# Kernel tuning notes

Measured on AMD Instinct MI355X. Metric: run time of the kernel, lower is better.

Reference implementation:

```python
import jax, jax.numpy as jnp
import numpy as np

DIM = 1024
NUM_HEADS = 16
HEAD_DIM = DIM // NUM_HEADS
SCALE = HEAD_DIM ** -0.5


def setup_inputs() -> dict:
    key = jax.random.key(0)
    ks = jax.random.split(key, 9)
    s = 0.02
    return {
        "x": jax.random.normal(ks[0], (4, 2048, DIM), dtype=jnp.float32),
        "Wq": jax.random.normal(ks[1], (DIM, DIM), dtype=jnp.float32) * s,
        "bq": jax.random.normal(ks[2], (DIM,), dtype=jnp.float32) * s,
        "Wk": jax.random.normal(ks[3], (DIM, DIM), dtype=jnp.float32) * s,
        "bk": jax.random.normal(ks[4], (DIM,), dtype=jnp.float32) * s,
        "Wv": jax.random.normal(ks[5], (DIM, DIM), dtype=jnp.float32) * s,
        "bv": jax.random.normal(ks[6], (DIM,), dtype=jnp.float32) * s,
        "Wo": jax.random.normal(ks[7], (DIM, DIM), dtype=jnp.float32) * s,
        "bo": jax.random.normal(ks[8], (DIM,), dtype=jnp.float32) * s,
    }


def reference(x, Wq, bq, Wk, bk, Wv, bv, Wo, bo):
    B, S, D = x.shape
    H, Dh = NUM_HEADS, HEAD_DIM

    def heads(t):  # [B,S,D] -> [B,H,S,Dh]
        return t.reshape(B, S, H, Dh).transpose(0, 2, 1, 3)

    q = heads(x @ Wq.T + bq)
    k = heads(x @ Wk.T + bk)
    v = heads(x @ Wv.T + bv)

    attn = jnp.einsum('bnqd,bnkd->bnqk', q, k) * SCALE
    attn = jax.nn.softmax(attn, axis=-1)
    out = jnp.einsum('bnqk,bnkd->bnqd', attn, v)  # [B,H,S,Dh]
    out = out.transpose(0, 2, 1, 3).reshape(B, S, D)
    return out @ Wo.T + bo
```

## Files before the change

kernel.cpp:

```cpp
#include <hip/hip_runtime.h>
#include <stdint.h>

#define DIMD 1024
#define NH   16
#define DH   64
#define BB   4
#define SS   2048
#define MTOT 8192

static constexpr float QSCALE = 0.18033688011112042f;

typedef unsigned short u16;
typedef __attribute__((ext_vector_type(8))) short bf8;
typedef __attribute__((ext_vector_type(4))) float f4;
typedef __attribute__((ext_vector_type(16))) float f16v;

#if __has_builtin(__builtin_amdgcn_exp2f)
#define EXP2(x) __builtin_amdgcn_exp2f(x)
#else
#define EXP2(x) exp2f(x)
#endif

__device__ inline u16 f2bf(float f) {
    union { float f; uint32_t u; } v; v.f = f;
    uint32_t r = v.u + 0x7fffu + ((v.u >> 16) & 1u);
    return (u16)(r >> 16);
}

__device__ inline void gld16(const void* g, void* l) {
    __builtin_amdgcn_global_load_lds(
        (const __attribute__((address_space(1))) uint32_t*)g,
        (__attribute__((address_space(3))) uint32_t*)l, 16, 0, 0);
}

__device__ inline uint32_t cvtpk(float lo, float hi) {
    uint32_t r;
    asm("v_cvt_pk_bf16_f32 %0, %1, %2" : "=v"(r) : "v"(lo), "v"(hi));
    return r;
}

__global__ void cvt_bf16(const float* __restrict__ src, u16* __restrict__ dst, int n) {
    int i = (blockIdx.x * blockDim.x + threadIdx.x) * 4;
    if (i >= n) return;
    float4 v = *(const float4*)(src + i);
    ushort4 o;
    o.x = f2bf(v.x); o.y = f2bf(v.y); o.z = f2bf(v.z); o.w = f2bf(v.w);
    *(ushort4*)(dst + i) = o;
}

__global__ __launch_bounds__(256, 2) void gemm_qkv(
    const u16* __restrict__ xb, const u16* __restrict__ Wb,
    const float* __restrict__ bq, const float* __restrict__ bk, const float* __restrict__ bv,
    u16* __restrict__ qkv, u16* __restrict__ vtb)
{
    __shared__ u16 lA[128 * 64];
    __shared__ u16 lB[128 * 64];
    const int tid = threadIdx.x;
    const int bm = blockIdx.x, bn = blockIdx.y, z = blockIdx.z;
    const u16* W = Wb + (size_t)z * DIMD * DIMD;
    const float* bias = (z == 0) ? bq : ((z == 1) ? bk : bv);
    u16* outp = qkv + (size_t)z * (size_t)MTOT * DIMD;

    const int lane = tid & 63, w = tid >> 6;
    const int wr = (w >> 1) * 64, wc = (w & 1) * 64;
    f4 acc[4][4] = {};

    const char* Abase = (const char*)xb + (size_t)(bm * 128) * 2048;
    const char* Bbase = (const char*)W + (size_t)(bn * 128) * 2048;

    for (int kt = 0; kt < 16; ++kt) {
        __syncthreads();
        #pragma unroll
        for (int p = 0; p < 4; ++p) {
            int off = (p * 256 + tid) * 16;
            int row = off >> 7, cb = off & 127;
            int scb = cb ^ ((row & 7) << 4);
            gld16(Abase + (size_t)row * 2048 + kt * 128 + scb, (char*)lA + off);
            gld16(Bbase + (size_t)row * 2048 + kt * 128 + scb, (char*)lB + off);
        }
        __syncthreads();
        #pragma unroll
        for (int ks = 0; ks < 2; ++ks) {
            const int cb = ks * 64 + ((lane >> 4) << 4);
            bf8 af[4], bfr[4];
            #pragma unroll
            for (int mi = 0; mi < 4; ++mi) {
                int r = wr + mi * 16 + (lane & 15);
                af[mi] = *(const bf8*)((const char*)lA + r * 128 + (cb ^ ((r & 7) << 4)));
            }
            #pragma unroll
            for (int ni = 0; ni < 4; ++ni) {
                int r = wc + ni * 16 + (lane & 15);
                bfr[ni] = *(const bf8*)((const char*)lB + r * 128 + (cb ^ ((r & 7) << 4)));
            }
            #pragma unroll
            for (int mi = 0; mi < 4; ++mi)
                #pragma unroll
                for (int ni = 0; ni < 4; ++ni)
                    acc[mi][ni] = __builtin_amdgcn_mfma_f32_16x16x32_bf16(af[mi], bfr[ni], acc[mi][ni], 0, 0, 0);
        }
    }

    if (z == 2) {
        #pragma unroll
        for (int ni = 0; ni < 4; ++ni) {
            int col = bn * 128 + wc + ni * 16 + (lane & 15);
            float bi = bias[col];
            int h = col >> 6, dh = col & 63;
            #pragma unroll
            for (int mi = 0; mi < 4; ++mi) {
                int row0 = bm * 128 + wr + mi * 16 + ((lane >> 4) << 2);
                int b = row0 >> 11, s = row0 & 2047;
                ushort4 st;
                st.x = f2bf(acc[mi][ni][0] + bi);
                st.y = f2bf(acc[mi][ni][1] + bi);
                st.z = f2bf(acc[mi][ni][2] + bi);
                st.w = f2bf(acc[mi][ni][3] + bi);
                *(ushort4*)(vtb + ((size_t)(b * NH + h) * DH + dh) * SS + s) = st;
            }
        }
    } else {
        const float mulv = (z == 0) ? QSCALE : 1.0f;
        #pragma unroll
        for (int ni = 0; ni < 4; ++ni) {
            int col = bn * 128 + wc + ni * 16 + (lane & 15);
            float bi = bias[col];
            int h = col >> 6, dh = col & 63;
            #pragma unroll
            for (int mi = 0; mi < 4; ++mi) {
                #pragma unroll
                for (int r = 0; r < 4; ++r) {
                    int row = bm * 128 + wr + mi * 16 + ((lane >> 4) << 2) + r;
                    int b = row >> 11, s = row & 2047;
                    outp[(((size_t)(b * NH + h) * SS + s) << 6) + dh] = f2bf((acc[mi][ni][r] + bi) * mulv);
                }
            }
        }
    }
}

__global__ __launch_bounds__(256, 2) void gemm_out(
    const u16* __restrict__ Ab, const u16* __restrict__ Wo,
    const float* __restrict__ bo, float* __restrict__ dout)
{
    __shared__ u16 lA[128 * 64];
    __shared__ u16 lB[128 * 64];
    const int tid = threadIdx.x;
    const int bm = blockIdx.x, bn = blockIdx.y;
    const int lane = tid & 63, w = tid >> 6;
    const int wr = (w >> 1) * 64, wc = (w & 1) * 64;
    f4 acc[4][4] = {};
    const char* Abase = (const char*)Ab + (size_t)(bm * 128) * 2048;
    const char* Bbase = (const char*)Wo + (size_t)(bn * 128) * 2048;

    for (int kt = 0; kt < 16; ++kt) {
        __syncthreads();
        #pragma unroll
        for (int p = 0; p < 4; ++p) {
            int off = (p * 256 + tid) * 16;
            int row = off >> 7, cb = off & 127;
            int scb = cb ^ ((row & 7) << 4);
            gld16(Abase + (size_t)row * 2048 + kt * 128 + scb, (char*)lA + off);
            gld16(Bbase + (size_t)row * 2048 + kt * 128 + scb, (char*)lB + off);
        }
        __syncthreads();
        #pragma unroll
        for (int ks = 0; ks < 2; ++ks) {
            const int cb = ks * 64 + ((lane >> 4) << 4);
            bf8 af[4], bfr[4];
            #pragma unroll
            for (int mi = 0; mi < 4; ++mi) {
                int r = wr + mi * 16 + (lane & 15);
                af[mi] = *(const bf8*)((const char*)lA + r * 128 + (cb ^ ((r & 7) << 4)));
            }
            #pragma unroll
            for (int ni = 0; ni < 4; ++ni) {
                int r = wc + ni * 16 + (lane & 15);
                bfr[ni] = *(const bf8*)((const char*)lB + r * 128 + (cb ^ ((r & 7) << 4)));
            }
            #pragma unroll
            for (int mi = 0; mi < 4; ++mi)
                #pragma unroll
                for (int ni = 0; ni < 4; ++ni)
                    acc[mi][ni] = __builtin_amdgcn_mfma_f32_16x16x32_bf16(af[mi], bfr[ni], acc[mi][ni], 0, 0, 0);
        }
    }
    #pragma unroll
    for (int ni = 0; ni < 4; ++ni) {
        int col = bn * 128 + wc + ni * 16 + (lane & 15);
        float bi = bo[col];
        #pragma unroll
        for (int mi = 0; mi < 4; ++mi) {
            #pragma unroll
            for (int r = 0; r < 4; ++r) {
                int row = bm * 128 + wr + mi * 16 + ((lane >> 4) << 2) + r;
                dout[(size_t)row * DIMD + col] = acc[mi][ni][r] + bi;
            }
        }
    }
}

__global__ __launch_bounds__(512, 2) void attn_fwd(
    const u16* __restrict__ Q, const u16* __restrict__ K,
    const u16* __restrict__ Vt, u16* __restrict__ O)
{
    __shared__ u16 lK[2][64 * 64];
    __shared__ u16 lV[2][64 * 64];

    const int tid = threadIdx.x;
    const int lane = tid & 63, w = tid >> 6;
    const int hi = lane >> 5, l31 = lane & 31;
    const int bh = blockIdx.y;
    const int qb0 = blockIdx.x * 256;
    const char* Kbase = (const char*)(K + (size_t)bh * SS * DH);
    const char* Vbase = (const char*)(Vt + (size_t)bh * DH * SS);

    const int qrow = qb0 + w * 32 + l31;
    const u16* Qp = Q + (size_t)bh * SS * DH + (size_t)qrow * DH;
    bf8 qf[4];
    #pragma unroll
    for (int kd = 0; kd < 4; ++kd)
        qf[kd] = *(const bf8*)(Qp + kd * 16 + hi * 8);

    f16v oacc0 = {}, oacc1 = {};
    float lsum = 0.f;

    auto stage = [&](int buf, int kv0) {
        int off = tid * 16;
        int row = off >> 7, cb = off & 127;
        int scb = cb ^ ((row & 7) << 4);
        gld16(Kbase + (size_t)(kv0 + row) * 128 + scb, (char*)lK[buf] + off);
        gld16(Vbase + (size_t)row * (SS * 2) + (size_t)kv0 * 2 + scb, (char*)lV[buf] + off);
    };

    stage(0, 0);
    __syncthreads();

    for (int it = 0; it < SS / 64; ++it) {
        const int cur = it & 1;
        if (it + 1 < SS / 64) stage(cur ^ 1, (it + 1) * 64);

        const char* lKc = (const char*)lK[cur];
        const char* lVc = (const char*)lV[cur];

        f16v s0 = {}, s1 = {};
        __builtin_amdgcn_s_setprio(1);
        #pragma unroll
        for (int kd = 0; kd < 4; ++kd) {
            const int colb = 32 * kd + 16 * hi;
            const int r0 = l31, r1 = 32 + l31;
            bf8 kf0 = *(const bf8*)(lKc + r0 * 128 + (colb ^ ((r0 & 7) << 4)));
            bf8 kf1 = *(const bf8*)(lKc + r1 * 128 + (colb ^ ((r1 & 7) << 4)));
            s0 = __builtin_amdgcn_mfma_f32_32x32x16_bf16(kf0, qf[kd], s0, 0, 0, 0);
            s1 = __builtin_amdgcn_mfma_f32_32x32x16_bf16(kf1, qf[kd], s1, 0, 0, 0);
        }
        __builtin_amdgcn_s_setprio(0);

        float ps[16];
        #pragma unroll
        for (int i = 0; i < 16; ++i) {
            float e0 = EXP2(s0[i]);
            float e1 = EXP2(s1[i]);
            s0[i] = e0; s1[i] = e1;
            ps[i] = e0 + e1;
        }
        float t0 = (ps[0] + ps[1]) + (ps[2] + ps[3]);
        float t1 = (ps[4] + ps[5]) + (ps[6] + ps[7]);
        float t2 = (ps[8] + ps[9]) + (ps[10] + ps[11]);
        float t3 = (ps[12] + ps[13]) + (ps[14] + ps[15]);
        lsum += (t0 + t1) + (t2 + t3);

        uint32_t wv0[8], wv1[8];
        #pragma unroll
        for (int a = 0; a < 4; ++a) {
            wv0[a * 2 + 0] = cvtpk(s0[4 * a + 0], s0[4 * a + 1]);
            wv0[a * 2 + 1] = cvtpk(s0[4 * a + 2], s0[4 * a + 3]);
            wv1[a * 2 + 0] = cvtpk(s1[4 * a + 0], s1[4 * a + 1]);
            wv1[a * 2 + 1] = cvtpk(s1[4 * a + 2], s1[4 * a + 3]);
        }

        #pragma unroll
        for (int ks = 0; ks < 4; ++ks) {
            const int kss = ks & 1;
            const uint32_t* wv = (ks < 2) ? wv0 : wv1;
            uint32_t w0 = wv[(2 * kss) * 2 + 0];
            uint32_t w1 = wv[(2 * kss) * 2 + 1];
            uint32_t w2 = wv[(2 * kss + 1) * 2 + 0];
            uint32_t w3 = wv[(2 * kss + 1) * 2 + 1];
            asm("v_permlane32_swap_b32 %0, %1" : "+v"(w0), "+v"(w2));
            asm("v_permlane32_swap_b32 %0, %1" : "+v"(w1), "+v"(w3));
            union { uint32_t u[4]; bf8 v; } pb;
            pb.u[0] = w0; pb.u[1] = w1; pb.u[2] = w2; pb.u[3] = w3;

            const int colb = 32 * ks + 16 * hi;
            const int r0 = l31, r1 = 32 + l31;
            bf8 vf0 = *(const bf8*)(lVc + r0 * 128 + (colb ^ ((r0 & 7) << 4)));
            bf8 vf1 = *(const bf8*)(lVc + r1 * 128 + (colb ^ ((r1 & 7) << 4)));
            __builtin_amdgcn_s_setprio(1);
            oacc0 = __builtin_amdgcn_mfma_f32_32x32x16_bf16(vf0, pb.v, oacc0, 0, 0, 0);
            oacc1 = __builtin_amdgcn_mfma_f32_32x32x16_bf16(vf1, pb.v, oacc1, 0, 0, 0);
            __builtin_amdgcn_s_setprio(0);
        }

        __syncthreads();
    }

    const float l = lsum + __shfl_xor(lsum, 32, 64);
    const int b = bh >> 4, h = bh & 15;
    const float inv = 1.f / l;
    u16* orow = O + (((size_t)(b * SS + qrow)) << 10) + h * DH;
    #pragma unroll
    for (int g = 0; g < 4; ++g) {
        ushort4 st0, st1;
        st0.x = f2bf(oacc0[4 * g + 0] * inv); st0.y = f2bf(oacc0[4 * g + 1] * inv);
        st0.z = f2bf(oacc0[4 * g + 2] * inv); st0.w = f2bf(oacc0[4 * g + 3] * inv);
        st1.x = f2bf(oacc1[4 * g + 0] * inv); st1.y = f2bf(oacc1[4 * g + 1] * inv);
        st1.z = f2bf(oacc1[4 * g + 2] * inv); st1.w = f2bf(oacc1[4 * g + 3] * inv);
        *(ushort4*)(orow + 8 * g + 4 * hi) = st0;
        *(ushort4*)(orow + 32 + 8 * g + 4 * hi) = st1;
    }
}

extern "C" void kernel_launch(void* const* d_in, const int* in_sizes, int n_in,
                              void* d_out, int out_size, void* d_ws, size_t ws_size,
                              hipStream_t stream) {
    const float* x  = (const float*)d_in[0];
    const float* Wq = (const float*)d_in[1];
    const float* bq = (const float*)d_in[2];
    const float* Wk = (const float*)d_in[3];
    const float* bk = (const float*)d_in[4];
    const float* Wv = (const float*)d_in[5];
    const float* bv = (const float*)d_in[6];
    const float* Wo = (const float*)d_in[7];
    const float* bo = (const float*)d_in[8];
    float* out = (float*)d_out;

    u16* wsp = (u16*)d_ws;
    const size_t NX = (size_t)MTOT * DIMD;
    const size_t NW = (size_t)DIMD * DIMD;
    u16* xb   = wsp;
    u16* Wb   = wsp + NX;
    u16* Qb   = wsp + NX + 4 * NW;
    u16* Kb   = Qb + NX;
    u16* Vtb  = Kb + NX;
    u16* attn = xb;

    cvt_bf16<<<dim3((int)(NX / 4 / 256)), 256, 0, stream>>>(x, xb, (int)NX);
    cvt_bf16<<<dim3((int)(NW / 4 / 256)), 256, 0, stream>>>(Wq, Wb + 0 * NW, (int)NW);
    cvt_bf16<<<dim3((int)(NW / 4 / 256)), 256, 0, stream>>>(Wk, Wb + 1 * NW, (int)NW);
    cvt_bf16<<<dim3((int)(NW / 4 / 256)), 256, 0, stream>>>(Wv, Wb + 2 * NW, (int)NW);
    cvt_bf16<<<dim3((int)(NW / 4 / 256)), 256, 0, stream>>>(Wo, Wb + 3 * NW, (int)NW);

    gemm_qkv<<<dim3(MTOT / 128, DIMD / 128, 3), 256, 0, stream>>>(xb, Wb, bq, bk, bv, Qb, Vtb);
    attn_fwd<<<dim3(SS / 256, BB * NH), 512, 0, stream>>>(Qb, Kb, Vtb, attn);
    gemm_out<<<dim3(MTOT / 128, DIMD / 128), 256, 0, stream>>>(attn, Wb + 3 * NW, bo, out);
}
```

Baseline: 185.7 us.

## Enlarge GEMM tiles with double-buffered LDS pipeline and give attention waves 64 query rows

```diff
diff --git a/kernel.cpp b/kernel.cpp
--- a/kernel.cpp
+++ b/kernel.cpp
@@ -20,6 +20,12 @@
 #else
 #define EXP2(x) exp2f(x)
 #endif
+
+#define SCHED0() __builtin_amdgcn_sched_barrier(0)
+#define BAR()  { SCHED0(); __builtin_amdgcn_s_barrier(); SCHED0(); }
+#define VM8()  { asm volatile("s_waitcnt vmcnt(8)" ::: "memory"); SCHED0(); }
+#define VM6()  { asm volatile("s_waitcnt vmcnt(6)" ::: "memory"); SCHED0(); }
+#define VM0()  { asm volatile("s_waitcnt vmcnt(0)" ::: "memory"); SCHED0(); }
 
 __device__ inline u16 f2bf(float f) {
     union { float f; uint32_t u; } v; v.f = f;
@@ -48,68 +54,112 @@
     *(ushort4*)(dst + i) = o;
 }
 
-__global__ __launch_bounds__(256, 2) void gemm_qkv(
+__global__ __launch_bounds__(512, 2) void gemm_qkv(
     const u16* __restrict__ xb, const u16* __restrict__ Wb,
     const float* __restrict__ bq, const float* __restrict__ bk, const float* __restrict__ bv,
     u16* __restrict__ qkv, u16* __restrict__ vtb)
 {
-    __shared__ u16 lA[128 * 64];
-    __shared__ u16 lB[128 * 64];
-    const int tid = threadIdx.x;
-    const int bm = blockIdx.x, bn = blockIdx.y, z = blockIdx.z;
+    __shared__ __align__(16) u16 lds[2][2][256 * 64];
+
+    int flat = blockIdx.x + 32 * blockIdx.y + 128 * blockIdx.z;
+    int swz = (flat & 7) * 48 + (flat >> 3);
+    int bm = swz & 31;
+    int j = swz >> 5;
+    int bn = j & 3, z = j >> 2;
+
     const u16* W = Wb + (size_t)z * DIMD * DIMD;
     const float* bias = (z == 0) ? bq : ((z == 1) ? bk : bv);
     u16* outp = qkv + (size_t)z * (size_t)MTOT * DIMD;
 
+    const int tid = threadIdx.x;
     const int lane = tid & 63, w = tid >> 6;
-    const int wr = (w >> 1) * 64, wc = (w & 1) * 64;
-    f4 acc[4][4] = {};
-
-    const char* Abase = (const char*)xb + (size_t)(bm * 128) * 2048;
-    const char* Bbase = (const char*)W + (size_t)(bn * 128) * 2048;
-
-    for (int kt = 0; kt < 16; ++kt) {
-        __syncthreads();
+    const int wr = (w >> 2) * 128, wc = (w & 3) * 64;
+
+    const char* Abase = (const char*)xb + (size_t)(bm * 256) * 2048;
+    const char* Bbase = (const char*)W + (size_t)(bn * 256) * 2048;
+
+    auto stage = [&](int t, int buf) {
         #pragma unroll
         for (int p = 0; p < 4; ++p) {
-            int off = (p * 256 + tid) * 16;
+            int off = (p * 512 + tid) * 16;
             int row = off >> 7, cb = off & 127;
             int scb = cb ^ ((row & 7) << 4);
-            gld16(Abase + (size_t)row * 2048 + kt * 128 + scb, (char*)lA + off);
-            gld16(Bbase + (size_t)row * 2048 + kt * 128 + scb, (char*)lB + off);
-        }
-        __syncthreads();
-        #pragma unroll
-        for (int ks = 0; ks < 2; ++ks) {
-            const int cb = ks * 64 + ((lane >> 4) << 4);
-            bf8 af[4], bfr[4];
-            #pragma unroll
-            for (int mi = 0; mi < 4; ++mi) {
-                int r = wr + mi * 16 + (lane & 15);
-                af[mi] = *(const bf8*)((const char*)lA + r * 128 + (cb ^ ((r & 7) << 4)));
-            }
-            #pragma unroll
-            for (int ni = 0; ni < 4; ++ni) {
-                int r = wc + ni * 16 + (lane & 15);
-                bfr[ni] = *(const bf8*)((const char*)lB + r * 128 + (cb ^ ((r & 7) << 4)));
-            }
-            #pragma unroll
-            for (int mi = 0; mi < 4; ++mi)
+            gld16(Abase + (size_t)row * 2048 + (size_t)t * 128 + scb, (char*)lds[buf][0] + off);
+            gld16(Bbase + (size_t)row * 2048 + (size_t)t * 128 + scb, (char*)lds[buf][1] + off);
+        }
+    };
+
+    f4 acc[8][4] = {};
+
+    stage(0, 0);
+    stage(1, 1);
+    VM8();
+    BAR();
+
+    for (int t = 0; t < 16; ++t) {
+        const char* lA = (const char*)lds[t & 1][0];
+        const char* lB = (const char*)lds[t & 1][1];
+        const int rswz = (lane & 7) << 4;
+        const int cb0 = ((lane >> 4) << 4);
+
+        bf8 bfr[4][2];
+        #pragma unroll
+        for (int ni = 0; ni < 4; ++ni) {
+            int r = wc + ni * 16 + (lane & 15);
+            #pragma unroll
+            for (int ks = 0; ks < 2; ++ks)
+                bfr[ni][ks] = *(const bf8*)(lB + r * 128 + ((ks * 64 + cb0) ^ rswz));
+        }
+        bf8 af[4][2];
+        #pragma unroll
+        for (int mi = 0; mi < 4; ++mi) {
+            int r = wr + mi * 16 + (lane & 15);
+            #pragma unroll
+            for (int ks = 0; ks < 2; ++ks)
+                af[mi][ks] = *(const bf8*)(lA + r * 128 + ((ks * 64 + cb0) ^ rswz));
+        }
+        __builtin_amdgcn_s_setprio(1);
+        #pragma unroll
+        for (int mi = 0; mi < 4; ++mi)
+            #pragma unroll
+            for (int ni = 0; ni < 4; ++ni)
                 #pragma unroll
-                for (int ni = 0; ni < 4; ++ni)
-                    acc[mi][ni] = __builtin_amdgcn_mfma_f32_16x16x32_bf16(af[mi], bfr[ni], acc[mi][ni], 0, 0, 0);
-        }
+                for (int ks = 0; ks < 2; ++ks)
+                    acc[mi][ni] = __builtin_amdgcn_mfma_f32_16x16x32_bf16(af[mi][ks], bfr[ni][ks], acc[mi][ni], 0, 0, 0);
+        __builtin_amdgcn_s_setprio(0);
+        #pragma unroll
+        for (int mi = 0; mi < 4; ++mi) {
+            int r = wr + 64 + mi * 16 + (lane & 15);
+            #pragma unroll
+            for (int ks = 0; ks < 2; ++ks)
+                af[mi][ks] = *(const bf8*)(lA + r * 128 + ((ks * 64 + cb0) ^ rswz));
+        }
+        __builtin_amdgcn_s_setprio(1);
+        #pragma unroll
+        for (int mi = 0; mi < 4; ++mi)
+            #pragma unroll
+            for (int ni = 0; ni < 4; ++ni)
+                #pragma unroll
+                for (int ks = 0; ks < 2; ++ks)
+                    acc[mi + 4][ni] = __builtin_amdgcn_mfma_f32_16x16x32_bf16(af[mi][ks], bfr[ni][ks], acc[mi + 4][ni], 0, 0, 0);
+        __builtin_amdgcn_s_setprio(0);
+
+        if (t == 15) break;
+        BAR();
+        if (t + 2 < 16) { stage(t + 2, t & 1); VM8(); }
+        else           { VM0(); }
+        BAR();
     }
 
     if (z == 2) {
         #pragma unroll
         for (int ni = 0; ni < 4; ++ni) {
-            int col = bn * 128 + wc + ni * 16 + (lane & 15);
+            int col = bn * 256 + wc + ni * 16 + (lane & 15);
             float bi = bias[col];
             int h = col >> 6, dh = col & 63;
             #pragma unroll
-            for (int mi = 0; mi < 4; ++mi) {
-                int row0 = bm * 128 + wr + mi * 16 + ((lane >> 4) << 2);
+            for (int mi = 0; mi < 8; ++mi) {
+                int row0 = bm * 256 + wr + mi * 16 + ((lane >> 4) << 2);
                 int b = row0 >> 11, s = row0 & 2047;
                 ushort4 st;
                 st.x = f2bf(acc[mi][ni][0] + bi);
@@ -123,14 +173,14 @@
         const float mulv = (z == 0) ? QSCALE : 1.0f;
         #pragma unroll
         for (int ni = 0; ni < 4; ++ni) {
-            int col = bn * 128 + wc + ni * 16 + (lane & 15);
+            int col = bn * 256 + wc + ni * 16 + (lane & 15);
             float bi = bias[col];
             int h = col >> 6, dh = col & 63;
             #pragma unroll
-            for (int mi = 0; mi < 4; ++mi) {
+            for (int mi = 0; mi < 8; ++mi) {
                 #pragma unroll
                 for (int r = 0; r < 4; ++r) {
-                    int row = bm * 128 + wr + mi * 16 + ((lane >> 4) << 2) + r;
+                    int row = bm * 256 + wr + mi * 16 + ((lane >> 4) << 2) + r;
                     int b = row >> 11, s = row & 2047;
                     outp[(((size_t)(b * NH + h) * SS + s) << 6) + dh] = f2bf((acc[mi][ni][r] + bi) * mulv);
                 }
@@ -139,52 +189,87 @@
     }
 }
 
-__global__ __launch_bounds__(256, 2) void gemm_out(
+__global__ __launch_bounds__(512, 2) void gemm_out(
     const u16* __restrict__ Ab, const u16* __restrict__ Wo,
     const float* __restrict__ bo, float* __restrict__ dout)
 {
-    __shared__ u16 lA[128 * 64];
-    __shared__ u16 lB[128 * 64];
+    __shared__ __align__(16) u16 lA[2][256 * 64];
+    __shared__ __align__(16) u16 lB[2][128 * 64];
+
+    int flat = blockIdx.x + 32 * blockIdx.y;
+    int swz = (flat & 7) * 32 + (flat >> 3);
+    int bm = swz & 31;
+    int bn = swz >> 5;
+
     const int tid = threadIdx.x;
-    const int bm = blockIdx.x, bn = blockIdx.y;
     const int lane = tid & 63, w = tid >> 6;
     const int wr = (w >> 1) * 64, wc = (w & 1) * 64;
-    f4 acc[4][4] = {};
-    const char* Abase = (const char*)Ab + (size_t)(bm * 128) * 2048;
+
+    const char* Abase = (const char*)Ab + (size_t)(bm * 256) * 2048;
     const char* Bbase = (const char*)Wo + (size_t)(bn * 128) * 2048;
 
-    for (int kt = 0; kt < 16; ++kt) {
-        __syncthreads();
+    auto stage = [&](int t, int buf) {
         #pragma unroll
         for (int p = 0; p < 4; ++p) {
-            int off = (p * 256 + tid) * 16;
+            int off = (p * 512 + tid) * 16;
             int row = off >> 7, cb = off & 127;
             int scb = cb ^ ((row & 7) << 4);
-            gld16(Abase + (size_t)row * 2048 + kt * 128 + scb, (char*)lA + off);
-            gld16(Bbase + (size_t)row * 2048 + kt * 128 + scb, (char*)lB + off);
-        }
-        __syncthreads();
-        #pragma unroll
-        for (int ks = 0; ks < 2; ++ks) {
-            const int cb = ks * 64 + ((lane >> 4) << 4);
-            bf8 af[4], bfr[4];
-            #pragma unroll
-            for (int mi = 0; mi < 4; ++mi) {
-                int r = wr + mi * 16 + (lane & 15);
-                af[mi] = *(const bf8*)((const char*)lA + r * 128 + (cb ^ ((r & 7) << 4)));
-            }
-            #pragma unroll
-            for (int ni = 0; ni < 4; ++ni) {
-                int r = wc + ni * 16 + (lane & 15);
-                bfr[ni] = *(const bf8*)((const char*)lB + r * 128 + (cb ^ ((r & 7) << 4)));
-            }
-            #pragma unroll
-            for (int mi = 0; mi < 4; ++mi)
+            gld16(Abase + (size_t)row * 2048 + (size_t)t * 128 + scb, (char*)lA[buf] + off);
+        }
+        #pragma unroll
+        for (int p = 0; p < 2; ++p) {
+            int off = (p * 512 + tid) * 16;
+            int row = off >> 7, cb = off & 127;
+            int scb = cb ^ ((row & 7) << 4);
+            gld16(Bbase + (size_t)row * 2048 + (size_t)t * 128 + scb, (char*)lB[buf] + off);
+        }
+    };
+
+    f4 acc[4][4] = {};
+
+    stage(0, 0);
+    stage(1, 1);
+    VM6();
+    BAR();
+
+    for (int t = 0; t < 16; ++t) {
+        const char* pA = (const char*)lA[t & 1];
+        const char* pB = (const char*)lB[t & 1];
+        const int rswz = (lane & 7) << 4;
+        const int cb0 = ((lane >> 4) << 4);
+
+        bf8 bfr[4][2], af[4][2];
+        #pragma unroll
+        for (int ni = 0; ni < 4; ++ni) {
+            int r = wc + ni * 16 + (lane & 15);
+            #pragma unroll
+            for (int ks = 0; ks < 2; ++ks)
+                bfr[ni][ks] = *(const bf8*)(pB + r * 128 + ((ks * 64 + cb0) ^ rswz));
+        }
+        #pragma unroll
+        for (int mi = 0; mi < 4; ++mi) {
+            int r = wr + mi * 16 + (lane & 15);
+            #pragma unroll
+            for (int ks = 0; ks < 2; ++ks)
+                af[mi][ks] = *(const bf8*)(pA + r * 128 + ((ks * 64 + cb0) ^ rswz));
+        }
+        __builtin_amdgcn_s_setprio(1);
+        #pragma unroll
+        for (int mi = 0; mi < 4; ++mi)
+            #pragma unroll
+            for (int ni = 0; ni < 4; ++ni)
                 #pragma unroll
-                for (int ni = 0; ni < 4; ++ni)
-                    acc[mi][ni] = __builtin_amdgcn_mfma_f32_16x16x32_bf16(af[mi], bfr[ni], acc[mi][ni], 0, 0, 0);
-        }
-    }
+                for (int ks = 0; ks < 2; ++ks)
+                    acc[mi][ni] = __builtin_amdgcn_mfma_f32_16x16x32_bf16(af[mi][ks], bfr[ni][ks], acc[mi][ni], 0, 0, 0);
+        __builtin_amdgcn_s_setprio(0);
+
+        if (t == 15) break;
+        BAR();
+        if (t + 2 < 16) { stage(t + 2, t & 1); VM6(); }
+        else           { VM0(); }
+        BAR();
+    }
+
     #pragma unroll
     for (int ni = 0; ni < 4; ++ni) {
         int col = bn * 128 + wc + ni * 16 + (lane & 15);
@@ -193,19 +278,19 @@
         for (int mi = 0; mi < 4; ++mi) {
             #pragma unroll
             for (int r = 0; r < 4; ++r) {
-                int row = bm * 128 + wr + mi * 16 + ((lane >> 4) << 2) + r;
+                int row = bm * 256 + wr + mi * 16 + ((lane >> 4) << 2) + r;
                 dout[(size_t)row * DIMD + col] = acc[mi][ni][r] + bi;
             }
         }
     }
 }
 
-__global__ __launch_bounds__(512, 2) void attn_fwd(
+__global__ __launch_bounds__(256, 2) void attn_fwd(
     const u16* __restrict__ Q, const u16* __restrict__ K,
     const u16* __restrict__ Vt, u16* __restrict__ O)
 {
-    __shared__ u16 lK[2][64 * 64];
-    __shared__ u16 lV[2][64 * 64];
+    __shared__ __align__(16) u16 lK[2][64 * 64];
+    __shared__ __align__(16) u16 lV[2][64 * 64];
 
     const int tid = threadIdx.x;
     const int lane = tid & 63, w = tid >> 6;
@@ -215,22 +300,28 @@
     const char* Kbase = (const char*)(K + (size_t)bh * SS * DH);
     const char* Vbase = (const char*)(Vt + (size_t)bh * DH * SS);
 
-    const int qrow = qb0 + w * 32 + l31;
-    const u16* Qp = Q + (size_t)bh * SS * DH + (size_t)qrow * DH;
-    bf8 qf[4];
+    const int q0 = qb0 + w * 64;
+    bf8 qf[2][4];
     #pragma unroll
-    for (int kd = 0; kd < 4; ++kd)
-        qf[kd] = *(const bf8*)(Qp + kd * 16 + hi * 8);
-
-    f16v oacc0 = {}, oacc1 = {};
-    float lsum = 0.f;
+    for (int qh = 0; qh < 2; ++qh) {
+        const u16* Qp = Q + (size_t)bh * SS * DH + (size_t)(q0 + qh * 32 + l31) * DH;
+        #pragma unroll
+        for (int kd = 0; kd < 4; ++kd)
+            qf[qh][kd] = *(const bf8*)(Qp + kd * 16 + hi * 8);
+    }
+
+    f16v oacc[2][2] = {};
+    float lsum[2] = {0.f, 0.f};
 
     auto stage = [&](int buf, int kv0) {
-        int off = tid * 16;
-        int row = off >> 7, cb = off & 127;
-        int scb = cb ^ ((row & 7) << 4);
-        gld16(Kbase + (size_t)(kv0 + row) * 128 + scb, (char*)lK[buf] + off);
-        gld16(Vbase + (size_t)row * (SS * 2) + (size_t)kv0 * 2 + scb, (char*)lV[buf] + off);
+        #pragma unroll
+        for (int p = 0; p < 2; ++p) {
+            int off = (p * 256 + tid) * 16;
+            int row = off >> 7, cb = off & 127;
+            int scb = cb ^ ((row & 7) << 4);
+            gld16(Kbase + (size_t)(kv0 + row) * 128 + scb, (char*)lK[buf] + off);
+            gld16(Vbase + (size_t)row * (SS * 2) + (size_t)kv0 * 2 + scb, (char*)lV[buf] + off);
+        }
     };
 
     stage(0, 0);
@@ -242,82 +333,97 @@
 
         const char* lKc = (const char*)lK[cur];
         const char* lVc = (const char*)lV[cur];
-
-        f16v s0 = {}, s1 = {};
+        const int rswz = (l31 & 7) << 4;
+
+        f16v s[2][2] = {};
         __builtin_amdgcn_s_setprio(1);
         #pragma unroll
         for (int kd = 0; kd < 4; ++kd) {
             const int colb = 32 * kd + 16 * hi;
-            const int r0 = l31, r1 = 32 + l31;
-            bf8 kf0 = *(const bf8*)(lKc + r0 * 128 + (colb ^ ((r0 & 7) << 4)));
-            bf8 kf1 = *(const bf8*)(lKc + r1 * 128 + (colb ^ ((r1 & 7) << 4)));
-            s0 = __builtin_amdgcn_mfma_f32_32x32x16_bf16(kf0, qf[kd], s0, 0, 0, 0);
-            s1 = __builtin_amdgcn_mfma_f32_32x32x16_bf16(kf1, qf[kd], s1, 0, 0, 0);
+            bf8 kf0 = *(const bf8*)(lKc + l31 * 128 + (colb ^ rswz));
+            bf8 kf1 = *(const bf8*)(lKc + (32 + l31) * 128 + (colb ^ rswz));
+            #pragma unroll
+            for (int qh = 0; qh < 2; ++qh) {
+                s[qh][0] = __builtin_amdgcn_mfma_f32_32x32x16_bf16(kf0, qf[qh][kd], s[qh][0], 0, 0, 0);
+                s[qh][1] = __builtin_amdgcn_mfma_f32_32x32x16_bf16(kf1, qf[qh][kd], s[qh][1], 0, 0, 0);
+            }
         }
         __builtin_amdgcn_s_setprio(0);
 
-        float ps[16];
-        #pragma unroll
-        for (int i = 0; i < 16; ++i) {
-            float e0 = EXP2(s0[i]);
-            float e1 = EXP2(s1[i]);
-            s0[i] = e0; s1[i] = e1;
-            ps[i] = e0 + e1;
-        }
-        float t0 = (ps[0] + ps[1]) + (ps[2] + ps[3]);
-        float t1 = (ps[4] + ps[5]) + (ps[6] + ps[7]);
-        float t2 = (ps[8] + ps[9]) + (ps[10] + ps[11]);
-        float t3 = (ps[12] + ps[13]) + (ps[14] + ps[15]);
-        lsum += (t0 + t1) + (t2 + t3);
-
-        uint32_t wv0[8], wv1[8];
-        #pragma unroll
-        for (int a = 0; a < 4; ++a) {
-            wv0[a * 2 + 0] = cvtpk(s0[4 * a + 0], s0[4 * a + 1]);
-            wv0[a * 2 + 1] = cvtpk(s0[4 * a + 2], s0[4 * a + 3]);
-            wv1[a * 2 + 0] = cvtpk(s1[4 * a + 0], s1[4 * a + 1]);
-            wv1[a * 2 + 1] = cvtpk(s1[4 * a + 2], s1[4 * a + 3]);
+        uint32_t wv[2][16];
+        #pragma unroll
+        for (int qh = 0; qh < 2; ++qh) {
+            float ps[16];
+            #pragma unroll
+            for (int i = 0; i < 16; ++i) {
+                float e0 = EXP2(s[qh][0][i]);
+                float e1 = EXP2(s[qh][1][i]);
+                s[qh][0][i] = e0; s[qh][1][i] = e1;
+                ps[i] = e0 + e1;
+            }
+            float t0 = (ps[0] + ps[1]) + (ps[2] + ps[3]);
+            float t1 = (ps[4] + ps[5]) + (ps[6] + ps[7]);
+            float t2 = (ps[8] + ps[9]) + (ps[10] + ps[11]);
+            float t3 = (ps[12] + ps[13]) + (ps[14] + ps[15]);
+            lsum[qh] += (t0 + t1) + (t2 + t3);
+            #pragma unroll
+            for (int a = 0; a < 4; ++a) {
+                wv[qh][a * 2 + 0] = cvtpk(s[qh][0][4 * a + 0], s[qh][0][4 * a + 1]);
+                wv[qh][a * 2 + 1] = cvtpk(s[qh][0][4 * a + 2], s[qh][0][4 * a + 3]);
+                wv[qh][8 + a * 2 + 0] = cvtpk(s[qh][1][4 * a + 0], s[qh][1][4 * a + 1]);
+                wv[qh][8 + a * 2 + 1] = cvtpk(s[qh][1][4 * a + 2], s[qh][1][4 * a + 3]);
+            }
         }
 
         #pragma unroll
         for (int ks = 0; ks < 4; ++ks) {
             const int kss = ks & 1;
-            const uint32_t* wv = (ks < 2) ? wv0 : wv1;
-            uint32_t w0 = wv[(2 * kss) * 2 + 0];
-            uint32_t w1 = wv[(2 * kss) * 2 + 1];
-            uint32_t w2 = wv[(2 * kss + 1) * 2 + 0];
-            uint32_t w3 = wv[(2 * kss + 1) * 2 + 1];
-            asm("v_permlane32_swap_b32 %0, %1" : "+v"(w0), "+v"(w2));
-            asm("v_permlane32_swap_b32 %0, %1" : "+v"(w1), "+v"(w3));
-            union { uint32_t u[4]; bf8 v; } pb;
-            pb.u[0] = w0; pb.u[1] = w1; pb.u[2] = w2; pb.u[3] = w3;
-
+            const int base = (ks < 2) ? 0 : 8;
+            bf8 pbv[2];
+            #pragma unroll
+            for (int qh = 0; qh < 2; ++qh) {
+                uint32_t w0 = wv[qh][base + 4 * kss + 0];
+                uint32_t w1 = wv[qh][base + 4 * kss + 1];
+                uint32_t w2 = wv[qh][base + 4 * kss + 2];
+                uint32_t w3 = wv[qh][base + 4 * kss + 3];
+                asm("v_permlane32_swap_b32 %0, %1" : "+v"(w0), "+v"(w2));
+                asm("v_permlane32_swap_b32 %0, %1" : "+v"(w1), "+v"(w3));
+                union { uint32_t u[4]; bf8 v; } pb;
+                pb.u[0] = w0; pb.u[1] = w1; pb.u[2] = w2; pb.u[3] = w3;
+                pbv[qh] = pb.v;
+            }
             const int colb = 32 * ks + 16 * hi;
-            const int r0 = l31, r1 = 32 + l31;
-            bf8 vf0 = *(const bf8*)(lVc + r0 * 128 + (colb ^ ((r0 & 7) << 4)));
-            bf8 vf1 = *(const bf8*)(lVc + r1 * 128 + (colb ^ ((r1 & 7) << 4)));
+            bf8 vf0 = *(const bf8*)(lVc + l31 * 128 + (colb ^ rswz));
+            bf8 vf1 = *(const bf8*)(lVc + (32 + l31) * 128 + (colb ^ rswz));
             __builtin_amdgcn_s_setprio(1);
-            oacc0 = __builtin_amdgcn_mfma_f32_32x32x16_bf16(vf0, pb.v, oacc0, 0, 0, 0);
-            oacc1 = __builtin_amdgcn_mfma_f32_32x32x16_bf16(vf1, pb.v, oacc1, 0, 0, 0);
+            #pragma unroll
+            for (int qh = 0; qh < 2; ++qh) {
+                oacc[qh][0] = __builtin_amdgcn_mfma_f32_32x32x16_bf16(vf0, pbv[qh], oacc[qh][0], 0, 0, 0);
+                oacc[qh][1] = __builtin_amdgcn_mfma_f32_32x32x16_bf16(vf1, pbv[qh], oacc[qh][1], 0, 0, 0);
+            }
             __builtin_amdgcn_s_setprio(0);
         }
 
         __syncthreads();
     }
 
-    const float l = lsum + __shfl_xor(lsum, 32, 64);
     const int b = bh >> 4, h = bh & 15;
-    const float inv = 1.f / l;
-    u16* orow = O + (((size_t)(b * SS + qrow)) << 10) + h * DH;
     #pragma unroll
-    for (int g = 0; g < 4; ++g) {
-        ushort4 st0, st1;
-        st0.x = f2bf(oacc0[4 * g + 0] * inv); st0.y = f2bf(oacc0[4 * g + 1] * inv);
-        st0.z = f2bf(oacc0[4 * g + 2] * inv); st0.w = f2bf(oacc0[4 * g + 3] * inv);
-        st1.x = f2bf(oacc1[4 * g + 0] * inv); st1.y = f2bf(oacc1[4 * g + 1] * inv);
-        st1.z = f2bf(oacc1[4 * g + 2] * inv); st1.w = f2bf(oacc1[4 * g + 3] * inv);
-        *(ushort4*)(orow + 8 * g + 4 * hi) = st0;
-        *(ushort4*)(orow + 32 + 8 * g + 4 * hi) = st1;
+    for (int qh = 0; qh < 2; ++qh) {
+        const float l = lsum[qh] + __shfl_xor(lsum[qh], 32, 64);
+        const float inv = 1.f / l;
+        const int q = q0 + qh * 32 + l31;
+        u16* orow = O + (((size_t)(b * SS + q)) << 10) + h * DH;
+        #pragma unroll
+        for (int g = 0; g < 4; ++g) {
+            ushort4 st0, st1;
+            st0.x = f2bf(oacc[qh][0][4 * g + 0] * inv); st0.y = f2bf(oacc[qh][0][4 * g + 1] * inv);
+            st0.z = f2bf(oacc[qh][0][4 * g + 2] * inv); st0.w = f2bf(oacc[qh][0][4 * g + 3] * inv);
+            st1.x = f2bf(oacc[qh][1][4 * g + 0] * inv); st1.y = f2bf(oacc[qh][1][4 * g + 1] * inv);
+            st1.z = f2bf(oacc[qh][1][4 * g + 2] * inv); st1.w = f2bf(oacc[qh][1][4 * g + 3] * inv);
+            *(ushort4*)(orow + 8 * g + 4 * hi) = st0;
+            *(ushort4*)(orow + 32 + 8 * g + 4 * hi) = st1;
+        }
     }
 }
 
@@ -351,7 +457,7 @@
     cvt_bf16<<<dim3((int)(NW / 4 / 256)), 256, 0, stream>>>(Wv, Wb + 2 * NW, (int)NW);
     cvt_bf16<<<dim3((int)(NW / 4 / 256)), 256, 0, stream>>>(Wo, Wb + 3 * NW, (int)NW);
 
-    gemm_qkv<<<dim3(MTOT / 128, DIMD / 128, 3), 256, 0, stream>>>(xb, Wb, bq, bk, bv, Qb, Vtb);
-    attn_fwd<<<dim3(SS / 256, BB * NH), 512, 0, stream>>>(Qb, Kb, Vtb, attn);
-    gemm_out<<<dim3(MTOT / 128, DIMD / 128), 256, 0, stream>>>(attn, Wb + 3 * NW, bo, out);
-}
+    gemm_qkv<<<dim3(32, 4, 3), 512, 0, stream>>>(xb, Wb, bq, bk, bv, Qb, Vtb);
+    attn_fwd<<<dim3(SS / 256, BB * NH), 256, 0, stream>>>(Qb, Kb, Vtb, attn);
+    gemm_out<<<dim3(32, 8), 512, 0, stream>>>(attn, Wb + 3 * NW, bo, out);
+}
```

Result: slower. 205.7 us (+10.7%).
